# Optimization experiments

Hardware: AMD Instinct MI355X
Metric: run time of the kernel (lower is better)

## Reference

```python
import jax, jax.numpy as jnp
import numpy as np
import math

B, T, D, H = 2, 2048, 1024, 16


def _layernorm(x, gamma, beta, eps=1e-5):
    mu = jnp.mean(x, axis=-1, keepdims=True)
    var = jnp.var(x, axis=-1, keepdims=True)
    return (x - mu) * jax.lax.rsqrt(var + eps) * gamma + beta


def setup_inputs() -> dict:
    key = jax.random.key(0)
    ks = jax.random.split(key, 12)
    s = 1.0 / math.sqrt(D)
    return {
        "x": jax.random.normal(ks[0], (B, T, D), dtype=jnp.float32),
        "src_mask": jax.random.randint(ks[1], (B, T, T), 0, 2, dtype=jnp.int32),
        "ln_gamma": jnp.ones((D,), jnp.float32),
        "ln_beta": jnp.zeros((D,), jnp.float32),
        "Wq": jax.random.normal(ks[2], (D, D), jnp.float32) * s,
        "bq": jnp.zeros((D,), jnp.float32),
        "Wk": jax.random.normal(ks[3], (D, D), jnp.float32) * s,
        "bk": jnp.zeros((D,), jnp.float32),
        "Wv": jax.random.normal(ks[4], (D, D), jnp.float32) * s,
        "bv": jnp.zeros((D,), jnp.float32),
        "Wo": jax.random.normal(ks[5], (D, D), jnp.float32) * s,
        "bo": jnp.zeros((D,), jnp.float32),
    }


def reference(x, src_mask, ln_gamma, ln_beta, Wq, bq, Wk, bk, Wv, bv, Wo, bo):
    Bx, Tx, Dx = x.shape
    dh = Dx // H
    xn = _layernorm(x, ln_gamma, ln_beta)  # single LN; the three calls are identical
    q = (xn @ Wq + bq).reshape(Bx, Tx, H, dh)
    k = (xn @ Wk + bk).reshape(Bx, Tx, H, dh)
    v = (xn @ Wv + bv).reshape(Bx, Tx, H, dh)
    # scores: B, n, m, h
    attn = jnp.einsum('bnhd,bmhd->bnmh', q, k) / math.sqrt(dh)
    attn = attn + (1.0 - src_mask.astype(attn.dtype))[..., None] * -100000.0
    weight = jax.nn.softmax(attn, axis=2)
    y = jnp.einsum('bnmh,bmhd->bnhd', weight, v).reshape(Bx, Tx, Dx)
    return x + (y @ Wo + bo)
```

## Files before the change

kernel.cpp:

```cpp
#include <hip/hip_runtime.h>
#include <hip/hip_bf16.h>
#include <stdint.h>

#define Tq 2048
#define Dd 1024
#define Hh 16

typedef unsigned short u16;
typedef __attribute__((ext_vector_type(8))) short short8;
typedef __attribute__((ext_vector_type(4))) float f32x4;

__device__ __forceinline__ u16 f2bf(float f) {
  union { float f; unsigned u; } v; v.f = f;
  unsigned r = (v.u + 0x7fffu + ((v.u >> 16) & 1u)) >> 16;
  return (u16)r;
}

__device__ __forceinline__ unsigned pk2bf(float a, float b) {
  __hip_bfloat162 h = __float22bfloat162_rn(float2{a, b});
  union { __hip_bfloat162 h; unsigned u; } c; c.h = h;
  return c.u;
}

__device__ __forceinline__ void load_lds16(const void* g, void* l) {
  __builtin_amdgcn_global_load_lds(
      (const __attribute__((address_space(1))) unsigned*)g,
      (__attribute__((address_space(3))) unsigned*)l, 16, 0, 0);
}

__device__ __forceinline__ f32x4 mfma16(short8 a, short8 b, f32x4 c) {
  return __builtin_amdgcn_mfma_f32_16x16x32_bf16(a, b, c, 0, 0, 0);
}

__global__ __launch_bounds__(256) void prep_kernel(
    const float* __restrict__ x, const float* __restrict__ gamma,
    const float* __restrict__ beta, u16* __restrict__ xn,
    const float* __restrict__ W0, const float* __restrict__ W1,
    const float* __restrict__ W2, const float* __restrict__ W3,
    u16* __restrict__ o_qkv, u16* __restrict__ o_o,
    const int* __restrict__ mask, uint32_t* __restrict__ bits,
    const float* __restrict__ bq, const float* __restrict__ bk,
    const float* __restrict__ bv, float* __restrict__ bias3) {
  __shared__ float t[32][33];
  int idx = blockIdx.x;
  int tid = threadIdx.x;
  if (idx < 4096) {
    int row = idx;
    const float4 v = ((const float4*)(x + (size_t)row * Dd))[tid];
    float s = v.x + v.y + v.z + v.w;
    float s2 = v.x * v.x + v.y * v.y + v.z * v.z + v.w * v.w;
#pragma unroll
    for (int off = 1; off < 64; off <<= 1) {
      s += __shfl_xor(s, off);
      s2 += __shfl_xor(s2, off);
    }
    int w = tid >> 6;
    if ((tid & 63) == 0) { t[0][w] = s; t[0][4 + w] = s2; }
    __syncthreads();
    s = t[0][0] + t[0][1] + t[0][2] + t[0][3];
    s2 = t[0][4] + t[0][5] + t[0][6] + t[0][7];
    float mu = s * (1.0f / Dd);
    float var = s2 * (1.0f / Dd) - mu * mu;
    float rstd = rsqrtf(var + 1e-5f);
    const float4 g = ((const float4*)gamma)[tid];
    const float4 bb = ((const float4*)beta)[tid];
    union { unsigned us[2]; uint2 u2; } o;
    o.us[0] = pk2bf((v.x - mu) * rstd * g.x + bb.x, (v.y - mu) * rstd * g.y + bb.y);
    o.us[1] = pk2bf((v.z - mu) * rstd * g.z + bb.z, (v.w - mu) * rstd * g.w + bb.w);
    *(uint2*)(xn + (size_t)row * Dd + tid * 4) = o.u2;
  } else if (idx < 8192) {
    int ti = idx - 4096;
    int z = ti >> 10, i = ti & 1023;
    const float* W = (z == 0) ? W0 : (z == 1) ? W1 : (z == 2) ? W2 : W3;
    u16* out = (z < 3) ? (o_qkv + (size_t)z * 1024 * 1024) : o_o;
    int k0 = (i & 31) * 32, n0 = (i >> 5) * 32;
    int tx = tid & 31, ty = tid >> 5;
#pragma unroll
    for (int j = 0; j < 4; ++j)
      t[ty + j * 8][tx] = W[(size_t)(k0 + ty + j * 8) * Dd + n0 + tx];
    __syncthreads();
#pragma unroll
    for (int j = 0; j < 4; ++j)
      out[(size_t)(n0 + ty + j * 8) * Dd + k0 + tx] = f2bf(t[tx][ty + j * 8]);
  } else if (idx < 9216) {
    int m = idx - 8192;
    int b = m >> 9, rest = m & 511;
    int qw = rest >> 3, kblk = rest & 7;
    int k = kblk * 256 + tid;
    const int* mp = mask + ((size_t)b * Tq + qw * 32) * Tq + k;
    uint32_t wv = 0;
#pragma unroll
    for (int j = 0; j < 32; ++j) wv |= (mp[(size_t)j * Tq] ? 1u : 0u) << j;
    bits[((size_t)b * 64 + qw) * Tq + k] = wv;
  } else {
    int i = (idx - 9216) * 256 + tid;
    float v = (i < 1024) ? bq[i] : (i < 2048) ? bk[i - 1024] : bv[i - 2048];
    bias3[i] = v;
  }
}

__global__ __launch_bounds__(256) void vt_kernel(
    const u16* __restrict__ qkv, u16* __restrict__ vt) {
  __shared__ u16 t[32][33];
  int bh = blockIdx.z;
  int b = bh >> 4, h = bh & 15;
  int t0 = blockIdx.x * 32, d0 = blockIdx.y * 32;
  int tx = threadIdx.x & 31, ty = threadIdx.x >> 5;
#pragma unroll
  for (int i = 0; i < 4; ++i)
    t[ty + i * 8][tx] =
        qkv[(size_t)(b * Tq + t0 + ty + i * 8) * 3072 + 2048 + h * 64 + d0 + tx];
  __syncthreads();
#pragma unroll
  for (int i = 0; i < 4; ++i)
    vt[((size_t)bh * 64 + d0 + ty + i * 8) * Tq + t0 + tx] = t[tx][ty + i * 8];
}

template <int MODE, int MT>
__global__ __launch_bounds__(256) void gemm_bt(
    const u16* __restrict__ A, const u16* __restrict__ Bt,
    const float* __restrict__ bias, const float* __restrict__ resid,
    void* __restrict__ Cout, int ldc, int K) {
  constexpr int MTI = MT / 32;
  __shared__ u16 As[MT * 64];
  __shared__ u16 Bs[128 * 64];
  int tid = threadIdx.x;
  int lane = tid & 63, w = tid >> 6;
  int l16 = lane & 15, quad = lane >> 4;
  int x7 = l16 & 7;
  int wm = w >> 1, wn = w & 1;
  int m0 = blockIdx.y * MT, n0 = blockIdx.x * 128;
  int r8 = lane >> 3;
  int phys = lane & 7;
  int chunk = phys ^ r8;
  const u16* ga0 = A + (size_t)(m0 + r8) * K + chunk * 8;
  const u16* gb0 = Bt + (size_t)(n0 + r8) * K + chunk * 8;
  f32x4 acc[MTI][4];
#pragma unroll
  for (int i = 0; i < MTI; ++i)
#pragma unroll
    for (int j = 0; j < 4; ++j) acc[i][j] = {0.f, 0.f, 0.f, 0.f};

  for (int k0 = 0; k0 < K; k0 += 64) {
    __syncthreads();
#pragma unroll
    for (int c = 0; c < MT / 32; ++c) {
      int rb = c * 32 + w * 8;
      load_lds16(ga0 + (size_t)rb * K + k0, (char*)As + rb * 128);
    }
#pragma unroll
    for (int c = 0; c < 4; ++c) {
      int rb = c * 32 + w * 8;
      load_lds16(gb0 + (size_t)rb * K + k0, (char*)Bs + rb * 128);
    }
    __syncthreads();
    short8 af[MTI][2], bf[4][2];
#pragma unroll
    for (int mt = 0; mt < MTI; ++mt) {
      int row = wm * (MT / 2) + mt * 16 + l16;
#pragma unroll
      for (int ks = 0; ks < 2; ++ks)
        af[mt][ks] = *(const short8*)&As[row * 64 + (((ks << 2) | quad) ^ x7) * 8];
    }
#pragma unroll
    for (int nt = 0; nt < 4; ++nt) {
      int row = wn * 64 + nt * 16 + l16;
#pragma unroll
      for (int ks = 0; ks < 2; ++ks)
        bf[nt][ks] = *(const short8*)&Bs[row * 64 + (((ks << 2) | quad) ^ x7) * 8];
    }
#pragma unroll
    for (int ks = 0; ks < 2; ++ks)
#pragma unroll
      for (int mt = 0; mt < MTI; ++mt)
#pragma unroll
        for (int nt = 0; nt < 4; ++nt)
          acc[mt][nt] = mfma16(af[mt][ks], bf[nt][ks], acc[mt][nt]);
  }
#pragma unroll
  for (int nt = 0; nt < 4; ++nt) {
    int col = n0 + wn * 64 + nt * 16 + l16;
    float bv = bias[col];
    float scl = (MODE == 0 && col < 1024) ? 0.18033688011112042f : 1.0f;
#pragma unroll
    for (int mt = 0; mt < MTI; ++mt) {
#pragma unroll
      for (int r = 0; r < 4; ++r) {
        int row = m0 + wm * (MT / 2) + mt * 16 + quad * 4 + r;
        size_t idx = (size_t)row * ldc + col;
        float vv = (acc[mt][nt][r] + bv) * scl;
        if (MODE == 0)
          ((u16*)Cout)[idx] = f2bf(vv);
        else
          ((float*)Cout)[idx] = vv + resid[idx];
      }
    }
  }
}

__global__ __launch_bounds__(256, 4) void attn_kernel(
    const u16* __restrict__ qkv, const u16* __restrict__ vt,
    const uint32_t* __restrict__ mbits, u16* __restrict__ ybuf) {
  __shared__ u16 Ks[2][64 * 64];
  __shared__ u16 Vs[2][64 * 64];
  __shared__ u16 Plds[4][16 * 64];
  int tid = threadIdx.x;
  int lane = tid & 63, w = tid >> 6;
  int l16 = lane & 15, quad = lane >> 4;
  int x7 = l16 & 7;
  int qt = blockIdx.x, h = blockIdx.y, b = blockIdx.z;
  int qbase = qt * 64 + w * 16;
  const u16* Qb = qkv + (size_t)b * Tq * 3072 + h * 64;
  const u16* Kb = Qb + 1024;
  const u16* Vb = vt + ((size_t)(b * Hh + h)) * 64 * Tq;
  const uint32_t* Mrow = mbits + ((size_t)b * 64 + (qbase >> 5)) * Tq;
  int shift = (w & 1) * 16 + l16;
  u16* Pw = Plds[w];

  int half = (w & 1) * 32;
  int r8 = lane >> 3;
  int phys = lane & 7;
  int chunk = phys ^ r8;
  bool isK = (w < 2);

  short8 qf[2];
#pragma unroll
  for (int ks = 0; ks < 2; ++ks)
    qf[ks] = *(const short8*)&Qb[(size_t)(qbase + l16) * 3072 + ks * 32 + quad * 8];

  f32x4 acc[4];
#pragma unroll
  for (int j = 0; j < 4; ++j) acc[j] = {0.f, 0.f, 0.f, 0.f};
  float lst = 0.f;

  auto stage = [&](int buf, int k0) {
    if (isK) {
#pragma unroll
      for (int j = 0; j < 4; ++j)
        load_lds16(Kb + (size_t)(k0 + half + j * 8 + r8) * 3072 + chunk * 8,
                   (char*)&Ks[buf][0] + (half + j * 8) * 128);
    } else {
#pragma unroll
      for (int j = 0; j < 4; ++j)
        load_lds16(Vb + (size_t)(half + j * 8 + r8) * Tq + k0 + chunk * 8,
                   (char*)&Vs[buf][0] + (half + j * 8) * 128);
    }
  };

  stage(0, 0);

  for (int kt = 0; kt < 32; ++kt) {
    int k0 = kt * 64;
    int buf = kt & 1;
    __syncthreads();
    uint32_t mv[4][4];
#pragma unroll
    for (int mt = 0; mt < 4; ++mt) {
      uint4 m4 = *(const uint4*)&Mrow[k0 + mt * 16 + quad * 4];
      mv[mt][0] = m4.x; mv[mt][1] = m4.y; mv[mt][2] = m4.z; mv[mt][3] = m4.w;
    }
    if (kt < 31) stage(buf ^ 1, k0 + 64);
    const u16* Kt = Ks[buf];
    const u16* Vtile = Vs[buf];
    f32x4 s[4];
#pragma unroll
    for (int i = 0; i < 4; ++i) s[i] = {0.f, 0.f, 0.f, 0.f};
#pragma unroll
    for (int mt = 0; mt < 4; ++mt)
#pragma unroll
      for (int ks = 0; ks < 2; ++ks) {
        short8 kf = *(const short8*)&Kt[(mt * 16 + l16) * 64 +
                                        (((ks << 2) | quad) ^ x7) * 8];
        s[mt] = mfma16(kf, qf[ks], s[mt]);
      }
#pragma unroll
    for (int mt = 0; mt < 4; ++mt) {
#pragma unroll
      for (int r = 0; r < 4; ++r) {
        float sv = ((mv[mt][r] >> shift) & 1u) ? s[mt][r] : -100000.0f;
        float p = exp2f(sv);
        s[mt][r] = p;
        lst += p;
      }
      union { unsigned us[2]; uint2 u2; } pk;
      pk.us[0] = pk2bf(s[mt][0], s[mt][1]);
      pk.us[1] = pk2bf(s[mt][2], s[mt][3]);
      int p16 = (mt * 2 + (quad >> 1)) ^ x7;
      *(uint2*)&Pw[l16 * 64 + p16 * 8 + (quad & 1) * 4] = pk.u2;
    }
    short8 pf[2];
#pragma unroll
    for (int ks = 0; ks < 2; ++ks)
      pf[ks] = *(const short8*)&Pw[l16 * 64 + (((ks << 2) | quad) ^ x7) * 8];
#pragma unroll
    for (int ks = 0; ks < 2; ++ks)
#pragma unroll
      for (int nt2 = 0; nt2 < 4; ++nt2) {
        short8 vf = *(const short8*)&Vtile[(nt2 * 16 + l16) * 64 +
                                           (((ks << 2) | quad) ^ x7) * 8];
        acc[nt2] = mfma16(pf[ks], vf, acc[nt2]);
      }
  }
  lst += __shfl_xor(lst, 16);
  lst += __shfl_xor(lst, 32);
#pragma unroll
  for (int r = 0; r < 4; ++r) {
    float li = 1.0f / __shfl(lst, quad * 4 + r);
    size_t row = (size_t)b * Tq + qbase + quad * 4 + r;
#pragma unroll
    for (int nt2 = 0; nt2 < 4; ++nt2)
      ybuf[row * Dd + h * 64 + nt2 * 16 + l16] = f2bf(acc[nt2][r] * li);
  }
}

extern "C" void kernel_launch(void* const* d_in, const int* in_sizes, int n_in,
                              void* d_out, int out_size, void* d_ws, size_t ws_size,
                              hipStream_t stream) {
  (void)in_sizes; (void)n_in; (void)out_size; (void)ws_size;
  const float* x = (const float*)d_in[0];
  const int* mask = (const int*)d_in[1];
  const float* gamma = (const float*)d_in[2];
  const float* beta = (const float*)d_in[3];
  const float* Wq = (const float*)d_in[4];
  const float* bq = (const float*)d_in[5];
  const float* Wk = (const float*)d_in[6];
  const float* bk = (const float*)d_in[7];
  const float* Wv = (const float*)d_in[8];
  const float* bv = (const float*)d_in[9];
  const float* Wo = (const float*)d_in[10];
  const float* bo = (const float*)d_in[11];
  float* out = (float*)d_out;
  char* ws = (char*)d_ws;

  constexpr size_t SZ_XN = (size_t)4096 * 1024 * 2;
  constexpr size_t SZ_WTQ = (size_t)3072 * 1024 * 2;
  constexpr size_t SZ_WOT = (size_t)1024 * 1024 * 2;
  constexpr size_t SZ_B3 = 3072 * 4;
  constexpr size_t SZ_QKV = (size_t)4096 * 3072 * 2;
  constexpr size_t SZ_MBITS = (size_t)2 * 64 * 2048 * 4;
  constexpr size_t SZ_VT = (size_t)2 * 16 * 64 * 2048 * 2;
  size_t off = 0;
  u16* xn = (u16*)(ws + off); off += SZ_XN;
  u16* wtqkv = (u16*)(ws + off); off += SZ_WTQ;
  u16* wot = (u16*)(ws + off); off += SZ_WOT;
  float* bias3 = (float*)(ws + off); off += SZ_B3;
  u16* qkvb = (u16*)(ws + off); off += SZ_QKV;
  uint32_t* mbits = (uint32_t*)(ws + off); off += SZ_MBITS;
  u16* vtb = (u16*)(ws + off); off += SZ_VT;
  u16* ybuf = (u16*)(ws + off);

  prep_kernel<<<dim3(9228), dim3(256), 0, stream>>>(
      x, gamma, beta, xn, Wq, Wk, Wv, Wo, wtqkv, wot, mask, mbits, bq, bk, bv,
      bias3);
  gemm_bt<0, 128><<<dim3(24, 32), dim3(256), 0, stream>>>(
      xn, wtqkv, bias3, nullptr, qkvb, 3072, 1024);
  vt_kernel<<<dim3(64, 2, 32), dim3(256), 0, stream>>>(qkvb, vtb);
  attn_kernel<<<dim3(32, 16, 2), dim3(256), 0, stream>>>(qkvb, vtb, mbits, ybuf);
  gemm_bt<1, 64><<<dim3(8, 64), dim3(256), 0, stream>>>(
      ybuf, wot, bo, x, out, 1024, 1024);
}
```

Measured before the change: 248.3 us.

## Fuse V transpose into QKV GEMM epilogue and keep P in registers

The QKV GEMM epilogue now writes the V columns directly in transposed per-head layout, so the separate vt_kernel launch and its extra read/write of V are gone. In the attention kernel the probability tile is no longer round-tripped through LDS. It is fed straight from registers into 16x16x16 bf16 MFMAs whose V fragment reads match the score accumulator layout. This removes one launch, LDS traffic and a dependency, but doubles the number of PV MFMA instructions, and the V epilogue stores are small scattered 8-byte writes.

```diff
diff --git a/kernel.cpp b/kernel.cpp
--- a/kernel.cpp
+++ b/kernel.cpp
@@ -8,6 +8,7 @@
 
 typedef unsigned short u16;
 typedef __attribute__((ext_vector_type(8))) short short8;
+typedef __attribute__((ext_vector_type(4))) short s16x4;
 typedef __attribute__((ext_vector_type(4))) float f32x4;
 
 __device__ __forceinline__ u16 f2bf(float f) {
@@ -28,8 +29,11 @@
       (__attribute__((address_space(3))) unsigned*)l, 16, 0, 0);
 }
 
-__device__ __forceinline__ f32x4 mfma16(short8 a, short8 b, f32x4 c) {
+__device__ __forceinline__ f32x4 mfma_k32(short8 a, short8 b, f32x4 c) {
   return __builtin_amdgcn_mfma_f32_16x16x32_bf16(a, b, c, 0, 0, 0);
+}
+__device__ __forceinline__ f32x4 mfma_k16(s16x4 a, s16x4 b, f32x4 c) {
+  return __builtin_amdgcn_mfma_f32_16x16x16bf16_1k(a, b, c, 0, 0, 0);
 }
 
 __global__ __launch_bounds__(256) void prep_kernel(
@@ -99,28 +103,11 @@
   }
 }
 
-__global__ __launch_bounds__(256) void vt_kernel(
-    const u16* __restrict__ qkv, u16* __restrict__ vt) {
-  __shared__ u16 t[32][33];
-  int bh = blockIdx.z;
-  int b = bh >> 4, h = bh & 15;
-  int t0 = blockIdx.x * 32, d0 = blockIdx.y * 32;
-  int tx = threadIdx.x & 31, ty = threadIdx.x >> 5;
-#pragma unroll
-  for (int i = 0; i < 4; ++i)
-    t[ty + i * 8][tx] =
-        qkv[(size_t)(b * Tq + t0 + ty + i * 8) * 3072 + 2048 + h * 64 + d0 + tx];
-  __syncthreads();
-#pragma unroll
-  for (int i = 0; i < 4; ++i)
-    vt[((size_t)bh * 64 + d0 + ty + i * 8) * Tq + t0 + tx] = t[tx][ty + i * 8];
-}
-
 template <int MODE, int MT>
 __global__ __launch_bounds__(256) void gemm_bt(
     const u16* __restrict__ A, const u16* __restrict__ Bt,
     const float* __restrict__ bias, const float* __restrict__ resid,
-    void* __restrict__ Cout, int ldc, int K) {
+    void* __restrict__ Cout, u16* __restrict__ vtout, int ldc, int K) {
   constexpr int MTI = MT / 32;
   __shared__ u16 As[MT * 64];
   __shared__ u16 Bs[128 * 64];
@@ -175,7 +162,7 @@
       for (int mt = 0; mt < MTI; ++mt)
 #pragma unroll
         for (int nt = 0; nt < 4; ++nt)
-          acc[mt][nt] = mfma16(af[mt][ks], bf[nt][ks], acc[mt][nt]);
+          acc[mt][nt] = mfma_k32(af[mt][ks], bf[nt][ks], acc[mt][nt]);
   }
 #pragma unroll
   for (int nt = 0; nt < 4; ++nt) {
@@ -184,15 +171,26 @@
     float scl = (MODE == 0 && col < 1024) ? 0.18033688011112042f : 1.0f;
 #pragma unroll
     for (int mt = 0; mt < MTI; ++mt) {
-#pragma unroll
-      for (int r = 0; r < 4; ++r) {
-        int row = m0 + wm * (MT / 2) + mt * 16 + quad * 4 + r;
-        size_t idx = (size_t)row * ldc + col;
-        float vv = (acc[mt][nt][r] + bv) * scl;
-        if (MODE == 0)
-          ((u16*)Cout)[idx] = f2bf(vv);
-        else
-          ((float*)Cout)[idx] = vv + resid[idx];
+      if (MODE == 0 && col >= 2048) {
+        int d9 = col - 2048;
+        int h = d9 >> 6, d = d9 & 63;
+        int t0 = m0 + wm * (MT / 2) + mt * 16 + quad * 4;
+        int b = t0 >> 11, tt = t0 & 2047;
+        union { unsigned us[2]; uint2 u2; } o;
+        o.us[0] = pk2bf(acc[mt][nt][0] + bv, acc[mt][nt][1] + bv);
+        o.us[1] = pk2bf(acc[mt][nt][2] + bv, acc[mt][nt][3] + bv);
+        *(uint2*)&vtout[((size_t)(b * Hh + h) * 64 + d) * Tq + tt] = o.u2;
+      } else {
+#pragma unroll
+        for (int r = 0; r < 4; ++r) {
+          int row = m0 + wm * (MT / 2) + mt * 16 + quad * 4 + r;
+          size_t idx = (size_t)row * ldc + col;
+          float vv = (acc[mt][nt][r] + bv) * scl;
+          if (MODE == 0)
+            ((u16*)Cout)[idx] = f2bf(vv);
+          else
+            ((float*)Cout)[idx] = vv + resid[idx];
+        }
       }
     }
   }
@@ -203,7 +201,6 @@
     const uint32_t* __restrict__ mbits, u16* __restrict__ ybuf) {
   __shared__ u16 Ks[2][64 * 64];
   __shared__ u16 Vs[2][64 * 64];
-  __shared__ u16 Plds[4][16 * 64];
   int tid = threadIdx.x;
   int lane = tid & 63, w = tid >> 6;
   int l16 = lane & 15, quad = lane >> 4;
@@ -215,7 +212,6 @@
   const u16* Vb = vt + ((size_t)(b * Hh + h)) * 64 * Tq;
   const uint32_t* Mrow = mbits + ((size_t)b * 64 + (qbase >> 5)) * Tq;
   int shift = (w & 1) * 16 + l16;
-  u16* Pw = Plds[w];
 
   int half = (w & 1) * 32;
   int r8 = lane >> 3;
@@ -271,8 +267,9 @@
       for (int ks = 0; ks < 2; ++ks) {
         short8 kf = *(const short8*)&Kt[(mt * 16 + l16) * 64 +
                                         (((ks << 2) | quad) ^ x7) * 8];
-        s[mt] = mfma16(kf, qf[ks], s[mt]);
+        s[mt] = mfma_k32(kf, qf[ks], s[mt]);
       }
+    s16x4 pfrag[4];
 #pragma unroll
     for (int mt = 0; mt < 4; ++mt) {
 #pragma unroll
@@ -282,24 +279,20 @@
         s[mt][r] = p;
         lst += p;
       }
-      union { unsigned us[2]; uint2 u2; } pk;
+      union { unsigned us[2]; s16x4 v; } pk;
       pk.us[0] = pk2bf(s[mt][0], s[mt][1]);
       pk.us[1] = pk2bf(s[mt][2], s[mt][3]);
-      int p16 = (mt * 2 + (quad >> 1)) ^ x7;
-      *(uint2*)&Pw[l16 * 64 + p16 * 8 + (quad & 1) * 4] = pk.u2;
-    }
-    short8 pf[2];
-#pragma unroll
-    for (int ks = 0; ks < 2; ++ks)
-      pf[ks] = *(const short8*)&Pw[l16 * 64 + (((ks << 2) | quad) ^ x7) * 8];
-#pragma unroll
-    for (int ks = 0; ks < 2; ++ks)
+      pfrag[mt] = pk.v;
+    }
+#pragma unroll
+    for (int mt = 0; mt < 4; ++mt) {
+      int vch = ((2 * mt + (quad >> 1)) ^ x7) * 8 + (quad & 1) * 4;
 #pragma unroll
       for (int nt2 = 0; nt2 < 4; ++nt2) {
-        short8 vf = *(const short8*)&Vtile[(nt2 * 16 + l16) * 64 +
-                                           (((ks << 2) | quad) ^ x7) * 8];
-        acc[nt2] = mfma16(pf[ks], vf, acc[nt2]);
+        s16x4 vf = *(const s16x4*)&Vtile[(nt2 * 16 + l16) * 64 + vch];
+        acc[nt2] = mfma_k16(pfrag[mt], vf, acc[nt2]);
       }
+    }
   }
   lst += __shfl_xor(lst, 16);
   lst += __shfl_xor(lst, 32);
@@ -353,9 +346,8 @@
       x, gamma, beta, xn, Wq, Wk, Wv, Wo, wtqkv, wot, mask, mbits, bq, bk, bv,
       bias3);
   gemm_bt<0, 128><<<dim3(24, 32), dim3(256), 0, stream>>>(
-      xn, wtqkv, bias3, nullptr, qkvb, 3072, 1024);
-  vt_kernel<<<dim3(64, 2, 32), dim3(256), 0, stream>>>(qkvb, vtb);
+      xn, wtqkv, bias3, nullptr, qkvb, vtb, 3072, 1024);
   attn_kernel<<<dim3(32, 16, 2), dim3(256), 0, stream>>>(qkvb, vtb, mbits, ybuf);
   gemm_bt<1, 64><<<dim3(8, 64), dim3(256), 0, stream>>>(
-      ybuf, wot, bo, x, out, 1024, 1024);
-}
+      ybuf, wot, bo, x, out, nullptr, 1024, 1024);
+}
```

Result: slower. 258.6 us (+4.1%).
